# Kernel tuning notes

Hardware: AMD Instinct MI355X
Metric: run time of the kernel (lower is better)

The kernel has to match this reference:

```python
import jax, jax.numpy as jnp
import numpy as np

NUM_HEADS = 12
ROPE_BASE = 10000.0


def _rope_cos_sin(n, head_dim):
    # inv_freq over even indices, emb = concat(freqs, freqs) as in standard RotaryEmbedding
    inv_freq = 1.0 / (ROPE_BASE ** (jnp.arange(0, head_dim, 2, dtype=jnp.float32) / head_dim))
    freqs = jnp.arange(n, dtype=jnp.float32)[:, None] * inv_freq[None, :]  # [n, hd/2]
    emb = jnp.concatenate([freqs, freqs], axis=-1)  # [n, hd]
    return jnp.cos(emb)[None, None], jnp.sin(emb)[None, None]  # [1,1,n,hd]


def _rotate_half(x):
    x1, x2 = jnp.split(x, 2, axis=-1)
    return jnp.concatenate([-x2, x1], axis=-1)


def setup_inputs() -> dict:
    key = jax.random.key(0)
    ks = jax.random.split(key, 6)
    B, Dq, T, Hp, Wp = 16, 768, 4, 16, 16
    Nt, Dkv = 64, 384
    return {
        "feat": jax.random.normal(ks[0], (B, Dq, T, Hp, Wp), jnp.float32),
        "tokens": jax.random.normal(ks[1], (B, Nt, Dkv), jnp.float32),
        "Wq": jax.random.normal(ks[2], (Dq, Dq), jnp.float32) * 0.02,
        "Wkv": jax.random.normal(ks[3], (Dkv, 2 * Dq), jnp.float32) * 0.02,
        "Wout": jax.random.normal(ks[4], (Dq, Dq), jnp.float32) * 0.02,
        "bout": jnp.zeros((Dq,), jnp.float32),
    }


def reference(feat, tokens, Wq, Wkv, Wout, bout):
    B, Dq, T, Hp, Wp = feat.shape
    H = NUM_HEADS
    hd = Dq // H
    Nq = T * Hp * Wp
    Nt = tokens.shape[1]
    scale = hd ** -0.5

    # q from feature map: flatten(2).transpose(1,2) -> [B, Nq, Dq]
    q_in = jnp.transpose(feat.reshape(B, Dq, Nq), (0, 2, 1))
    q = q_in @ Wq                      # [B, Nq, Dq]
    kv = tokens @ Wkv                  # [B, Nt, 2*Dq]
    k, v = jnp.split(kv, 2, axis=-1)

    def to_heads(x, n):
        return jnp.transpose(x.reshape(B, n, H, hd), (0, 2, 1, 3))  # [B,H,n,hd]

    q = to_heads(q, Nq)
    k = to_heads(k, Nt)
    v = to_heads(v, Nt)

    cos_q, sin_q = _rope_cos_sin(Nq, hd)
    cos_k, sin_k = _rope_cos_sin(Nt, hd)
    q = q * cos_q + _rotate_half(q) * sin_q
    k = k * cos_k + _rotate_half(k) * sin_k

    attn = jax.nn.softmax(jnp.einsum("bhqd,bhkd->bhqk", q, k) * scale, axis=-1)
    out = jnp.einsum("bhqk,bhkd->bhqd", attn, v)           # [B,H,Nq,hd]
    out = jnp.transpose(out, (0, 2, 1, 3)).reshape(B, Nq, Dq)
    out = out @ Wout + bout
    out = jnp.transpose(out, (0, 2, 1)).reshape(B, Dq, T, Hp, Wp)
    return feat + out
```

## Files before the change

kernel.cpp:

```cpp
#include <hip/hip_runtime.h>
#include <stdint.h>

#define BATCH 16
#define DQ 768
#define NQ 1024
#define NT 64
#define DKV 384
#define NHEAD 12
#define HD 64
#define HD2 32

typedef __attribute__((ext_vector_type(8))) short bf16x8;
typedef __attribute__((ext_vector_type(4))) float f32x4;

__device__ __forceinline__ unsigned short f2bf(float f) {
    unsigned u = __float_as_uint(f);
    u += 0x7fff + ((u >> 16) & 1);
    return (unsigned short)(u >> 16);
}
__device__ __forceinline__ float bf2f(unsigned short h) {
    return __uint_as_float((unsigned)h << 16);
}

__device__ __forceinline__ void gload_lds16(const void* g, void* l) {
    __builtin_amdgcn_global_load_lds(
        (const __attribute__((address_space(1))) unsigned int*)g,
        (__attribute__((address_space(3))) unsigned int*)l, 16, 0, 0);
}

__global__ __launch_bounds__(256) void conv_feat_k(const float* __restrict__ feat,
                                                   unsigned short* __restrict__ featT) {
    const int b = blockIdx.z;
    const int n0 = blockIdx.x * 64;
    const int c0 = blockIdx.y * 64;
    __shared__ float T[64][65];
    const int tid = threadIdx.x;
    const int r = tid >> 4, c4 = (tid & 15) * 4;
    const float* fb = feat + (size_t)b * DQ * NQ + (size_t)c0 * NQ + n0;
    for (int rr = 0; rr < 64; rr += 16) {
        float4 v = *(const float4*)(fb + (size_t)(rr + r) * NQ + c4);
        T[rr + r][c4 + 0] = v.x; T[rr + r][c4 + 1] = v.y;
        T[rr + r][c4 + 2] = v.z; T[rr + r][c4 + 3] = v.w;
    }
    __syncthreads();
    unsigned short* ob = featT + ((size_t)b * NQ + n0) * DQ + c0;
    for (int rr = 0; rr < 64; rr += 16) {
        int dr = rr + r;
        ushort4 w;
        w.x = f2bf(T[c4 + 0][dr]); w.y = f2bf(T[c4 + 1][dr]);
        w.z = f2bf(T[c4 + 2][dr]); w.w = f2bf(T[c4 + 3][dr]);
        *(ushort4*)(ob + (size_t)dr * DQ + c4) = w;
    }
}

__global__ __launch_bounds__(256) void conv_w_k(const float* __restrict__ Wq,
                                                const float* __restrict__ Wout,
                                                unsigned short* __restrict__ WqT,
                                                unsigned short* __restrict__ WoutT) {
    const float* src = blockIdx.z ? Wout : Wq;
    unsigned short* dst = blockIdx.z ? WoutT : WqT;
    const int r0 = blockIdx.x * 64;
    const int c0 = blockIdx.y * 64;
    __shared__ float T[64][65];
    const int tid = threadIdx.x;
    const int r = tid >> 4, c4 = (tid & 15) * 4;
    for (int rr = 0; rr < 64; rr += 16) {
        float4 v = *(const float4*)(src + (size_t)(r0 + rr + r) * DQ + c0 + c4);
        T[rr + r][c4 + 0] = v.x; T[rr + r][c4 + 1] = v.y;
        T[rr + r][c4 + 2] = v.z; T[rr + r][c4 + 3] = v.w;
    }
    __syncthreads();
    for (int rr = 0; rr < 64; rr += 16) {
        int dr = rr + r;
        ushort4 w;
        w.x = f2bf(T[c4 + 0][dr]); w.y = f2bf(T[c4 + 1][dr]);
        w.z = f2bf(T[c4 + 2][dr]); w.w = f2bf(T[c4 + 3][dr]);
        *(ushort4*)(dst + (size_t)(c0 + dr) * DQ + r0 + c4) = w;
    }
}

__global__ __launch_bounds__(256) void gemm_kv_k(const float* __restrict__ tokens,
                                                 const float* __restrict__ Wkv,
                                                 float* __restrict__ kv_out) {
    const int b = blockIdx.z;
    const int j0 = blockIdx.x * 64;
    __shared__ float As[16][64];
    __shared__ float Bs[16][64];
    const int tid = threadIdx.x;
    const int tx = tid & 15, ty = tid >> 4;
    float acc[4][4] = {};
    const float* tb = tokens + (size_t)b * NT * DKV;
    for (int c0 = 0; c0 < DKV; c0 += 16) {
        {
            int m = tid >> 2, jq = tid & 3;
            float4 v = *(const float4*)(tb + (size_t)m * DKV + c0 + jq * 4);
            As[jq * 4 + 0][m] = v.x; As[jq * 4 + 1][m] = v.y;
            As[jq * 4 + 2][m] = v.z; As[jq * 4 + 3][m] = v.w;
            int kk = tid >> 4, n4 = (tid & 15) * 4;
            *(float4*)&Bs[kk][n4] = *(const float4*)(Wkv + (size_t)(c0 + kk) * (2 * DQ) + j0 + n4);
        }
        __syncthreads();
#pragma unroll
        for (int kk = 0; kk < 16; ++kk) {
            float a[4], bb[4];
            *(float4*)a  = *(float4*)&As[kk][ty * 4];
            *(float4*)bb = *(float4*)&Bs[kk][tx * 4];
#pragma unroll
            for (int i = 0; i < 4; ++i)
#pragma unroll
                for (int j = 0; j < 4; ++j)
                    acc[i][j] += a[i] * bb[j];
        }
        __syncthreads();
    }
    float* ob = kv_out + (size_t)b * NT * (2 * DQ);
#pragma unroll
    for (int i = 0; i < 4; ++i)
        *(float4*)(ob + (size_t)(ty * 4 + i) * (2 * DQ) + j0 + tx * 4) = *(float4*)acc[i];
}

__global__ __launch_bounds__(256) void gemm_q_mfma(const unsigned short* __restrict__ At,
                                                   const unsigned short* __restrict__ Bt,
                                                   unsigned short* __restrict__ C) {
    const int b = blockIdx.z;
    const int m0 = blockIdx.x * 128;
    const int n0 = blockIdx.y * 128;
    __shared__ __align__(16) unsigned short ldsA[2][128 * 32];
    __shared__ __align__(16) unsigned short ldsB[2][128 * 32];
    const int tid = threadIdx.x;
    const int lane = tid & 63;
    const int wm = ((tid >> 7) & 1) * 64;
    const int wn = ((tid >> 6) & 1) * 64;
    const int fr = lane & 15;
    const int fg = lane >> 4;
    const int pslot = (fg ^ ((fr >> 1) & 3)) * 16;
    const int wbase = (tid & 192) * 16;
    f32x4 acc[4][4] = {};

    const unsigned short* Ab = At + (size_t)b * NQ * DQ + (size_t)m0 * DQ;
    const unsigned short* Bb = Bt + (size_t)n0 * DQ;
    const int srow_lo = tid >> 2;
    const int sslot = tid & 3;

    auto STAGE = [&](int buf, int k0) {
#pragma unroll
        for (int i = 0; i < 2; ++i) {
            int row = i * 64 + srow_lo;
            int sl = sslot ^ ((row >> 1) & 3);
            gload_lds16(Ab + (size_t)row * DQ + k0 + sl * 8,
                        (char*)ldsA[buf] + i * 4096 + wbase);
            gload_lds16(Bb + (size_t)row * DQ + k0 + sl * 8,
                        (char*)ldsB[buf] + i * 4096 + wbase);
        }
    };

    STAGE(0, 0);
    __syncthreads();
    int cur = 0;
    const int NSTEP = DQ / 32;
    for (int t = 0; t < NSTEP; ++t) {
        if (t + 1 < NSTEP) STAGE(cur ^ 1, (t + 1) * 32);
        bf16x8 af[4], bfr[4];
#pragma unroll
        for (int f = 0; f < 4; ++f) {
            af[f]  = *(const bf16x8*)((const char*)ldsA[cur] + (wm + f * 16 + fr) * 64 + pslot);
            bfr[f] = *(const bf16x8*)((const char*)ldsB[cur] + (wn + f * 16 + fr) * 64 + pslot);
        }
#pragma unroll
        for (int i = 0; i < 4; ++i)
#pragma unroll
            for (int j = 0; j < 4; ++j)
                acc[i][j] = __builtin_amdgcn_mfma_f32_16x16x32_bf16(af[i], bfr[j], acc[i][j], 0, 0, 0);
        __syncthreads();
        cur ^= 1;
    }
    unsigned short* Cb = C + (size_t)b * NQ * DQ;
#pragma unroll
    for (int i = 0; i < 4; ++i)
#pragma unroll
        for (int j = 0; j < 4; ++j) {
            int rbase = m0 + wm + i * 16 + fg * 4;
            int col = n0 + wn + j * 16 + fr;
#pragma unroll
            for (int r = 0; r < 4; ++r)
                Cb[(size_t)(rbase + r) * DQ + col] = f2bf(acc[i][j][r]);
        }
}

__global__ __launch_bounds__(256) void gemm_out_mfma(const unsigned short* __restrict__ At,
                                                     const unsigned short* __restrict__ Bt,
                                                     const float* __restrict__ feat,
                                                     const float* __restrict__ bout,
                                                     float* __restrict__ out) {
    const int b = blockIdx.z;
    const int m0 = blockIdx.x * 128;
    const int n0 = blockIdx.y * 128;
    __shared__ __align__(16) unsigned short ldsA[2][128 * 32];
    __shared__ __align__(16) unsigned short ldsB[2][128 * 32];
    const int tid = threadIdx.x;
    const int lane = tid & 63;
    const int wm = ((tid >> 7) & 1) * 64;
    const int wn = ((tid >> 6) & 1) * 64;
    const int fr = lane & 15;
    const int fg = lane >> 4;
    const int pslot = (fg ^ ((fr >> 1) & 3)) * 16;
    const int wbase = (tid & 192) * 16;
    f32x4 acc[4][4] = {};

    const unsigned short* Ab = At + (size_t)m0 * DQ;
    const unsigned short* Bb = Bt + (size_t)b * NQ * DQ + (size_t)n0 * DQ;
    const int srow_lo = tid >> 2;
    const int sslot = tid & 3;

    auto STAGE = [&](int buf, int k0) {
#pragma unroll
        for (int i = 0; i < 2; ++i) {
            int row = i * 64 + srow_lo;
            int sl = sslot ^ ((row >> 1) & 3);
            gload_lds16(Ab + (size_t)row * DQ + k0 + sl * 8,
                        (char*)ldsA[buf] + i * 4096 + wbase);
            gload_lds16(Bb + (size_t)row * DQ + k0 + sl * 8,
                        (char*)ldsB[buf] + i * 4096 + wbase);
        }
    };

    STAGE(0, 0);
    __syncthreads();
    int cur = 0;
    const int NSTEP = DQ / 32;
    for (int t = 0; t < NSTEP; ++t) {
        if (t + 1 < NSTEP) STAGE(cur ^ 1, (t + 1) * 32);
        bf16x8 af[4], bfr[4];
#pragma unroll
        for (int f = 0; f < 4; ++f) {
            af[f]  = *(const bf16x8*)((const char*)ldsA[cur] + (wm + f * 16 + fr) * 64 + pslot);
            bfr[f] = *(const bf16x8*)((const char*)ldsB[cur] + (wn + f * 16 + fr) * 64 + pslot);
        }
#pragma unroll
        for (int i = 0; i < 4; ++i)
#pragma unroll
            for (int j = 0; j < 4; ++j)
                acc[i][j] = __builtin_amdgcn_mfma_f32_16x16x32_bf16(af[i], bfr[j], acc[i][j], 0, 0, 0);
        __syncthreads();
        cur ^= 1;
    }
    float* ob = out + (size_t)b * DQ * NQ;
    const float* fb = feat + (size_t)b * DQ * NQ;
#pragma unroll
    for (int i = 0; i < 4; ++i)
#pragma unroll
        for (int j = 0; j < 4; ++j) {
            int dbase = m0 + wm + i * 16 + fg * 4;
            int n = n0 + wn + j * 16 + fr;
#pragma unroll
            for (int r = 0; r < 4; ++r) {
                int d = dbase + r;
                size_t idx = (size_t)d * NQ + n;
                ob[idx] = acc[i][j][r] + fb[idx] + bout[d];
            }
        }
}

__global__ __launch_bounds__(256) void attn_mfma(const float* __restrict__ kv,
                                                 unsigned short* __restrict__ q) {
    const int qb = blockIdx.x, h = blockIdx.y, b = blockIdx.z;
    const int n0 = qb * 256;
    __shared__ __align__(16) unsigned short Ks[64][72];
    __shared__ __align__(16) unsigned short VT[64][72];
    __shared__ __align__(16) unsigned short Ps[4][16][72];
    const int tid = threadIdx.x;
    const int lane = tid & 63;
    const int wid = tid >> 6;
    const int fr = lane & 15;
    const int fg = lane >> 4;

    {
        const int t = tid >> 2, dg = (tid & 3) * 8;
        const float* krow = kv + ((size_t)b * NT + t) * (2 * DQ) + h * HD;
        float lo[8], hi[8];
        *(float4*)&lo[0] = *(const float4*)(krow + dg);
        *(float4*)&lo[4] = *(const float4*)(krow + dg + 4);
        *(float4*)&hi[0] = *(const float4*)(krow + dg + 32);
        *(float4*)&hi[4] = *(const float4*)(krow + dg + 36);
        union { bf16x8 v; unsigned short u[8]; } plo, phi;
#pragma unroll
        for (int e = 0; e < 8; ++e) {
            float inv = exp2f((float)(dg + e) * -0.41524101186092029f);
            float s, c; __sincosf((float)t * inv, &s, &c);
            plo.u[e] = f2bf(lo[e] * c - hi[e] * s);
            phi.u[e] = f2bf(hi[e] * c + lo[e] * s);
        }
        *(bf16x8*)&Ks[t][dg]      = plo.v;
        *(bf16x8*)&Ks[t][dg + 32] = phi.v;
    }
    {
        const int t = tid >> 2, d0 = (tid & 3) * 16;
        const float* vrow = kv + ((size_t)b * NT + t) * (2 * DQ) + DQ + h * HD + d0;
        float vv[16];
        *(float4*)&vv[0]  = *(const float4*)(vrow + 0);
        *(float4*)&vv[4]  = *(const float4*)(vrow + 4);
        *(float4*)&vv[8]  = *(const float4*)(vrow + 8);
        *(float4*)&vv[12] = *(const float4*)(vrow + 12);
#pragma unroll
        for (int dd = 0; dd < 16; ++dd)
            VT[d0 + dd][t] = f2bf(vv[dd]);
    }
    __syncthreads();

    bf16x8 kf[4][2], vf[4][2];
#pragma unroll
    for (int j = 0; j < 4; ++j)
#pragma unroll
        for (int hh = 0; hh < 2; ++hh) {
            kf[j][hh] = *(const bf16x8*)&Ks[j * 16 + fr][hh * 32 + fg * 8];
            vf[j][hh] = *(const bf16x8*)&VT[j * 16 + fr][hh * 32 + fg * 8];
        }

    float invf[8];
#pragma unroll
    for (int e = 0; e < 8; ++e)
        invf[e] = exp2f((float)(fg * 8 + e) * -0.41524101186092029f);

    unsigned short* qbase = q + ((size_t)b * NQ + n0) * DQ + h * HD;

    for (int rt = wid; rt < 16; rt += 4) {
        const int row = rt * 16 + fr;
        const unsigned short* qrow = qbase + (size_t)row * DQ + fg * 8;
        bf16x8 q0 = *(const bf16x8*)qrow;
        bf16x8 q1 = *(const bf16x8*)(qrow + 32);
        union { bf16x8 v; unsigned short u[8]; } qa, qb2;
        const float pos = (float)(n0 + row);
#pragma unroll
        for (int e = 0; e < 8; ++e) {
            float s, c; __sincosf(pos * invf[e], &s, &c);
            float v0 = bf2f((unsigned short)q0[e]);
            float v1 = bf2f((unsigned short)q1[e]);
            qa.u[e]  = f2bf((v0 * c - v1 * s) * 0.125f);
            qb2.u[e] = f2bf((v1 * c + v0 * s) * 0.125f);
        }
        f32x4 sc[4];
#pragma unroll
        for (int j = 0; j < 4; ++j) {
            f32x4 z = {};
            sc[j] = __builtin_amdgcn_mfma_f32_16x16x32_bf16(qa.v, kf[j][0], z, 0, 0, 0);
            sc[j] = __builtin_amdgcn_mfma_f32_16x16x32_bf16(qb2.v, kf[j][1], sc[j], 0, 0, 0);
        }
#pragma unroll
        for (int r = 0; r < 4; ++r) {
            float m = fmaxf(fmaxf(sc[0][r], sc[1][r]), fmaxf(sc[2][r], sc[3][r]));
            for (int off = 1; off < 16; off <<= 1) m = fmaxf(m, __shfl_xor(m, off));
            float s = 0.f;
#pragma unroll
            for (int j = 0; j < 4; ++j) { float p = __expf(sc[j][r] - m); sc[j][r] = p; s += p; }
            for (int off = 1; off < 16; off <<= 1) s += __shfl_xor(s, off);
            float is = 1.0f / s;
#pragma unroll
            for (int j = 0; j < 4; ++j) sc[j][r] *= is;
        }
#pragma unroll
        for (int r = 0; r < 4; ++r)
#pragma unroll
            for (int j = 0; j < 4; ++j)
                Ps[wid][fg * 4 + r][j * 16 + fr] = f2bf(sc[j][r]);
        bf16x8 pa0 = *(const bf16x8*)&Ps[wid][fr][fg * 8];
        bf16x8 pa1 = *(const bf16x8*)&Ps[wid][fr][32 + fg * 8];
#pragma unroll
        for (int n = 0; n < 4; ++n) {
            f32x4 z = {};
            f32x4 o = __builtin_amdgcn_mfma_f32_16x16x32_bf16(pa0, vf[n][0], z, 0, 0, 0);
            o = __builtin_amdgcn_mfma_f32_16x16x32_bf16(pa1, vf[n][1], o, 0, 0, 0);
#pragma unroll
            for (int r = 0; r < 4; ++r)
                Ps[wid][fg * 4 + r][n * 16 + fr] = f2bf(o[r]);
        }
#pragma unroll
        for (int p = 0; p < 2; ++p) {
            int rr = p * 8 + (lane >> 3), ch = lane & 7;
            bf16x8 ov = *(const bf16x8*)&Ps[wid][rr][ch * 8];
            *(bf16x8*)(qbase + (size_t)(rt * 16 + rr) * DQ + ch * 8) = ov;
        }
    }
}

extern "C" void kernel_launch(void* const* d_in, const int* in_sizes, int n_in,
                              void* d_out, int out_size, void* d_ws, size_t ws_size,
                              hipStream_t stream) {
    const float* feat   = (const float*)d_in[0];
    const float* tokens = (const float*)d_in[1];
    const float* Wq     = (const float*)d_in[2];
    const float* Wkv    = (const float*)d_in[3];
    const float* Wout   = (const float*)d_in[4];
    const float* bout   = (const float*)d_in[5];
    float* out = (float*)d_out;

    float* ws_kv = (float*)d_ws;
    unsigned short* ws_featT = (unsigned short*)(ws_kv + (size_t)BATCH * NT * 2 * DQ);
    unsigned short* ws_q     = ws_featT + (size_t)BATCH * NQ * DQ;
    unsigned short* ws_WqT   = ws_q + (size_t)BATCH * NQ * DQ;
    unsigned short* ws_WoutT = ws_WqT + (size_t)DQ * DQ;

    conv_w_k<<<dim3(12, 12, 2), 256, 0, stream>>>(Wq, Wout, ws_WqT, ws_WoutT);
    conv_feat_k<<<dim3(16, 12, BATCH), 256, 0, stream>>>(feat, ws_featT);
    gemm_kv_k<<<dim3(24, 1, BATCH), 256, 0, stream>>>(tokens, Wkv, ws_kv);
    gemm_q_mfma<<<dim3(8, 6, BATCH), 256, 0, stream>>>(ws_featT, ws_WqT, ws_q);
    attn_mfma<<<dim3(4, 12, BATCH), 256, 0, stream>>>(ws_kv, ws_q);
    gemm_out_mfma<<<dim3(6, 8, BATCH), 256, 0, stream>>>(ws_WoutT, ws_q, feat, bout, out);
}
```

Before: 230.0 us.

## Triple-buffer LDS staging in Q and output GEMMs with one barrier per step

Both MFMA GEMM kernels move from double to triple buffering of the LDS tiles. Loads are issued two K-steps ahead, and each step waits with a partial vmcnt before a single s_barrier, replacing the two __syncthreads per iteration. This is meant to hide global-load latency and cut synchronization. The cost is 50% more LDS per block, which may reduce occupancy, plus reliance on hand-counted vmcnt values for correctness.

```diff
diff --git a/kernel.cpp b/kernel.cpp
--- a/kernel.cpp
+++ b/kernel.cpp
@@ -125,8 +125,8 @@
     const int b = blockIdx.z;
     const int m0 = blockIdx.x * 128;
     const int n0 = blockIdx.y * 128;
-    __shared__ __align__(16) unsigned short ldsA[2][128 * 32];
-    __shared__ __align__(16) unsigned short ldsB[2][128 * 32];
+    __shared__ __align__(16) unsigned short ldsA[3][128 * 32];
+    __shared__ __align__(16) unsigned short ldsB[3][128 * 32];
     const int tid = threadIdx.x;
     const int lane = tid & 63;
     const int wm = ((tid >> 7) & 1) * 64;
@@ -154,12 +154,20 @@
         }
     };
 
+    const int NSTEP = DQ / 32;
     STAGE(0, 0);
-    __syncthreads();
+    STAGE(1, 32);
     int cur = 0;
-    const int NSTEP = DQ / 32;
     for (int t = 0; t < NSTEP; ++t) {
-        if (t + 1 < NSTEP) STAGE(cur ^ 1, (t + 1) * 32);
+        if (t + 1 < NSTEP) {
+            asm volatile("s_waitcnt vmcnt(4)" ::: "memory");
+        } else {
+            asm volatile("s_waitcnt vmcnt(0)" ::: "memory");
+        }
+        __builtin_amdgcn_s_barrier();
+        __builtin_amdgcn_sched_barrier(0);
+        int nxt = cur + 2; if (nxt >= 3) nxt -= 3;
+        if (t + 2 < NSTEP) STAGE(nxt, (t + 2) * 32);
         bf16x8 af[4], bfr[4];
 #pragma unroll
         for (int f = 0; f < 4; ++f) {
@@ -171,8 +179,7 @@
 #pragma unroll
             for (int j = 0; j < 4; ++j)
                 acc[i][j] = __builtin_amdgcn_mfma_f32_16x16x32_bf16(af[i], bfr[j], acc[i][j], 0, 0, 0);
-        __syncthreads();
-        cur ^= 1;
+        cur = cur + 1; if (cur >= 3) cur = 0;
     }
     unsigned short* Cb = C + (size_t)b * NQ * DQ;
 #pragma unroll
@@ -195,8 +202,8 @@
     const int b = blockIdx.z;
     const int m0 = blockIdx.x * 128;
     const int n0 = blockIdx.y * 128;
-    __shared__ __align__(16) unsigned short ldsA[2][128 * 32];
-    __shared__ __align__(16) unsigned short ldsB[2][128 * 32];
+    __shared__ __align__(16) unsigned short ldsA[3][128 * 32];
+    __shared__ __align__(16) unsigned short ldsB[3][128 * 32];
     const int tid = threadIdx.x;
     const int lane = tid & 63;
     const int wm = ((tid >> 7) & 1) * 64;
@@ -224,12 +231,20 @@
         }
     };
 
+    const int NSTEP = DQ / 32;
     STAGE(0, 0);
-    __syncthreads();
+    STAGE(1, 32);
     int cur = 0;
-    const int NSTEP = DQ / 32;
     for (int t = 0; t < NSTEP; ++t) {
-        if (t + 1 < NSTEP) STAGE(cur ^ 1, (t + 1) * 32);
+        if (t + 1 < NSTEP) {
+            asm volatile("s_waitcnt vmcnt(4)" ::: "memory");
+        } else {
+            asm volatile("s_waitcnt vmcnt(0)" ::: "memory");
+        }
+        __builtin_amdgcn_s_barrier();
+        __builtin_amdgcn_sched_barrier(0);
+        int nxt = cur + 2; if (nxt >= 3) nxt -= 3;
+        if (t + 2 < NSTEP) STAGE(nxt, (t + 2) * 32);
         bf16x8 af[4], bfr[4];
 #pragma unroll
         for (int f = 0; f < 4; ++f) {
@@ -241,8 +256,7 @@
 #pragma unroll
             for (int j = 0; j < 4; ++j)
                 acc[i][j] = __builtin_amdgcn_mfma_f32_16x16x32_bf16(af[i], bfr[j], acc[i][j], 0, 0, 0);
-        __syncthreads();
-        cur ^= 1;
+        cur = cur + 1; if (cur >= 3) cur = 0;
     }
     float* ob = out + (size_t)b * DQ * NQ;
     const float* fb = feat + (size_t)b * DQ * NQ;
```

Result: faster. 222.8 us (-3.1%).
